# Performance work log

Hardware: AMD Instinct MI355X
Metric: run time of the kernel (lower is better)

Reference implementation:

```python
import jax, jax.numpy as jnp
import numpy as np

EPS = 1e-3  # Keras LayerNormalization default epsilon


def setup_inputs() -> dict:
    key = jax.random.key(0)
    ks = jax.random.split(key, 10)
    B, S, D, U = 4, 4096, 1024, 1024
    sc_in = 1.0 / np.sqrt(D)
    sc_u = 1.0 / np.sqrt(U)
    return {
        "inputs": jax.random.normal(ks[0], (B, S, D), dtype=jnp.float32),
        "w1": jax.random.normal(ks[1], (D, U), dtype=jnp.float32) * sc_in,
        "b1": jnp.zeros((U,), dtype=jnp.float32),
        "w2": jax.random.normal(ks[2], (U, U), dtype=jnp.float32) * sc_u,
        "b2": jnp.zeros((U,), dtype=jnp.float32),
        "wg": jax.random.normal(ks[3], (D, U), dtype=jnp.float32) * sc_in,
        "bg": jnp.zeros((U,), dtype=jnp.float32),
        "ws": jax.random.normal(ks[4], (D, U), dtype=jnp.float32) * sc_in,
        "bs": jnp.zeros((U,), dtype=jnp.float32),
        "gamma": jnp.ones((U,), dtype=jnp.float32),
        "beta": jnp.zeros((U,), dtype=jnp.float32),
    }


def reference(inputs, w1, b1, w2, b2, wg, bg, ws, bs, gamma, beta):
    # hidden branch: Dense(relu) -> (dropout inactive at inference) -> Dense
    h = jax.nn.relu(jnp.einsum('bsd,du->bsu', inputs, w1) + b1)
    x = jnp.einsum('bsu,uv->bsv', h, w2) + b2
    # gate on raw inputs
    g = jax.nn.sigmoid(jnp.einsum('bsd,du->bsu', inputs, wg) + bg)
    # skip projection
    s = jnp.einsum('bsd,du->bsu', inputs, ws) + bs
    y = x * g + s
    # LayerNormalization over last axis (Keras default eps=1e-3)
    mu = jnp.mean(y, axis=-1, keepdims=True)
    var = jnp.mean(jnp.square(y - mu), axis=-1, keepdims=True)
    return (y - mu) * jax.lax.rsqrt(var + EPS) * gamma + beta
```

## Files before the change

### kernel.cpp

```cpp
#include <hip/hip_runtime.h>
#include <hip/hip_bf16.h>

typedef short short8 __attribute__((ext_vector_type(8)));
typedef float f32x4 __attribute__((ext_vector_type(4)));

#define M_TOT 16384
#define NDIM  1024
#define BM 256
#define BN 256
#define BK 64
#define KH 32
#define NT (NDIM / BK)

static __device__ __forceinline__ unsigned short f2bf(float f) {
  unsigned int u = __builtin_bit_cast(unsigned int, f);
  unsigned int r = (u + 0x7fffu + ((u >> 16) & 1u)) >> 16;
  return (unsigned short)r;
}
static __device__ __forceinline__ float bf2f(unsigned short u) {
  return __builtin_bit_cast(float, ((unsigned int)u) << 16);
}

#define CLB() asm volatile("" ::: "memory")

__global__ __launch_bounds__(256) void cast_in(const float* __restrict__ in,
                                               unsigned short* __restrict__ out,
                                               int n4) {
  int i = blockIdx.x * 256 + threadIdx.x;
  if (i >= n4) return;
  float4 v = reinterpret_cast<const float4*>(in)[i];
  ushort4 o;
  o.x = f2bf(v.x); o.y = f2bf(v.y); o.z = f2bf(v.z); o.w = f2bf(v.w);
  reinterpret_cast<ushort4*>(out)[i] = o;
}

__global__ __launch_bounds__(256) void tcast(const float* __restrict__ src,
                                             unsigned short* __restrict__ dst) {
  __shared__ unsigned short tile[32][33];
  int bx = blockIdx.x * 32, by = blockIdx.y * 32;
  int x = threadIdx.x & 31, y = threadIdx.x >> 5;
#pragma unroll
  for (int i = 0; i < 32; i += 8)
    tile[y + i][x] = f2bf(src[(size_t)(by + y + i) * NDIM + bx + x]);
  __syncthreads();
#pragma unroll
  for (int i = 0; i < 32; i += 8)
    dst[(size_t)(bx + y + i) * NDIM + by + x] = tile[x][y + i];
}

template <int MODE>
__global__ __launch_bounds__(512, 2) void gemm256(
    const unsigned short* __restrict__ A,
    const unsigned short* __restrict__ Bt,
    const float* __restrict__ bias,
    unsigned short* __restrict__ O,
    const unsigned short* __restrict__ G,
    const unsigned short* __restrict__ S) {
  __shared__ __align__(16) unsigned short lds[2][2][2][256][KH];

  const int tid = threadIdx.x;
  const int lane = tid & 63;
  const int wave = tid >> 6;
  const int wm = wave >> 2;
  const int wn = wave & 3;

  const int id = blockIdx.x;
  const int xcd = id & 7;
  const int slot = id >> 3;
  const int rblk = xcd + 8 * (slot >> 2);
  const int cblk = slot & 3;
  const int m0 = rblk * BM, n0 = cblk * BN;

  const unsigned short* gA = A + (size_t)m0 * NDIM;
  const unsigned short* gB = Bt + (size_t)n0 * NDIM;

  f32x4 acc[8][4] = {};

  auto stage = [&](int buf, int mat, int h, const unsigned short* gsrc, int kt) {
#pragma unroll
    for (int j = 0; j < 2; ++j) {
      int cid = j * 512 + tid;
      int row = cid >> 2;
      int cs = cid & 3;
      int c = cs ^ ((row >> 1) & 3);
      const unsigned short* g = gsrc + (size_t)row * NDIM + kt * BK + h * KH + c * 8;
      unsigned short* l = &lds[buf][mat][h][0][0] + (size_t)(j * 512 + (tid & ~63)) * 8;
      __builtin_amdgcn_global_load_lds(
          (__attribute__((address_space(1))) void*)g,
          (__attribute__((address_space(3))) void*)l, 16, 0, 0);
    }
  };

  auto ldA = [&](short8* dst, int buf, int mih, int kk) {
#pragma unroll
    for (int mi = 0; mi < 4; ++mi) {
      int row = wm * 128 + (mih * 4 + mi) * 16 + (lane & 15);
      int cs = (lane >> 4) ^ ((row >> 1) & 3);
      dst[mi] = *reinterpret_cast<const short8*>(&lds[buf][0][kk][row][cs * 8]);
    }
  };
  auto ldB = [&](short8* dst, int buf, int kk) {
#pragma unroll
    for (int nj = 0; nj < 4; ++nj) {
      int row = wn * 64 + nj * 16 + (lane & 15);
      int cs = (lane >> 4) ^ ((row >> 1) & 3);
      dst[nj] = *reinterpret_cast<const short8*>(&lds[buf][1][kk][row][cs * 8]);
    }
  };

#define MFMA_Q(A4, B4, MI0)                                               \
  do {                                                                    \
    _Pragma("unroll") for (int mi = 0; mi < 4; ++mi)                      \
    _Pragma("unroll") for (int nj = 0; nj < 4; ++nj)                      \
      acc[MI0 + mi][nj] = __builtin_amdgcn_mfma_f32_16x16x32_bf16(        \
          A4[mi], B4[nj], acc[MI0 + mi][nj], 0, 0, 0);                    \
  } while (0)

#define BAR() do { CLB(); __builtin_amdgcn_s_barrier(); CLB(); } while (0)

  stage(0, 0, 0, gA, 0);
  stage(0, 1, 0, gB, 0);
  stage(0, 0, 1, gA, 0);
  stage(0, 1, 1, gB, 0);
  asm volatile("s_waitcnt vmcnt(4)" ::: "memory");
  BAR();

  short8 a_[4], b0_[4], b1_[4];

#pragma unroll 2
  for (int t = 0; t < NT; ++t) {
    const int cur = t & 1, nxt = cur ^ 1;
    const int ktn = (t < NT - 1) ? t + 1 : t;

    stage(nxt, 0, 0, gA, ktn);
    ldA(a_, cur, 0, 0);
    ldB(b0_, cur, 0);
    BAR();
    __builtin_amdgcn_s_setprio(1);
    MFMA_Q(a_, b0_, 0);
    __builtin_amdgcn_s_setprio(0);
    BAR();

    stage(nxt, 1, 0, gB, ktn);
    ldA(a_, cur, 1, 0);
    BAR();
    __builtin_amdgcn_s_setprio(1);
    MFMA_Q(a_, b0_, 4);
    __builtin_amdgcn_s_setprio(0);
    asm volatile("s_waitcnt vmcnt(4)" ::: "memory");
    BAR();

    stage(nxt, 0, 1, gA, ktn);
    ldA(a_, cur, 0, 1);
    ldB(b1_, cur, 1);
    BAR();
    __builtin_amdgcn_s_setprio(1);
    MFMA_Q(a_, b1_, 0);
    __builtin_amdgcn_s_setprio(0);
    BAR();

    stage(nxt, 1, 1, gB, ktn);
    ldA(a_, cur, 1, 1);
    BAR();
    __builtin_amdgcn_s_setprio(1);
    MFMA_Q(a_, b1_, 4);
    __builtin_amdgcn_s_setprio(0);
    asm volatile("s_waitcnt vmcnt(4)" ::: "memory");
    BAR();
  }

  const int crow0 = m0 + wm * 128;
  const int ccol0 = n0 + wn * 64;
#pragma unroll
  for (int mi = 0; mi < 8; ++mi) {
#pragma unroll
    for (int nj = 0; nj < 4; ++nj) {
      int row = crow0 + mi * 16 + ((lane >> 4) << 2);
      int col = ccol0 + nj * 16 + (lane & 15);
      float bc = bias[col];
#pragma unroll
      for (int r = 0; r < 4; ++r) {
        float v = acc[mi][nj][r] + bc;
        size_t idx = (size_t)(row + r) * NDIM + col;
        if (MODE == 0) {
          O[idx] = f2bf(fmaxf(v, 0.f));
        } else if (MODE == 1) {
          O[idx] = f2bf(1.f / (1.f + __expf(-v)));
        } else if (MODE == 2) {
          O[idx] = f2bf(v);
        } else {
          O[idx] = f2bf(v * bf2f(G[idx]) + bf2f(S[idx]));
        }
      }
    }
  }
#undef MFMA_Q
#undef BAR
}

__global__ __launch_bounds__(256) void layernorm_bf(
    const unsigned short* __restrict__ Ybf, float* __restrict__ Out,
    const float* __restrict__ gamma, const float* __restrict__ beta) {
  const int tid = threadIdx.x;
  const unsigned short* y = Ybf + (size_t)blockIdx.x * NDIM;
  ushort4 u = reinterpret_cast<const ushort4*>(y)[tid];
  float v0 = bf2f(u.x), v1 = bf2f(u.y), v2 = bf2f(u.z), v3 = bf2f(u.w);
  float s1 = v0 + v1 + v2 + v3;
  float s2 = v0 * v0 + v1 * v1 + v2 * v2 + v3 * v3;
#pragma unroll
  for (int o = 32; o > 0; o >>= 1) {
    s1 += __shfl_down(s1, o, 64);
    s2 += __shfl_down(s2, o, 64);
  }
  __shared__ float red[8];
  int wave = tid >> 6, lane = tid & 63;
  if (lane == 0) { red[wave] = s1; red[wave + 4] = s2; }
  __syncthreads();
  float S1 = red[0] + red[1] + red[2] + red[3];
  float S2 = red[4] + red[5] + red[6] + red[7];
  float mu = S1 * (1.f / NDIM);
  float var = S2 * (1.f / NDIM) - mu * mu;
  float inv = rsqrtf(var + 1e-3f);
  float4 gm = reinterpret_cast<const float4*>(gamma)[tid];
  float4 bt = reinterpret_cast<const float4*>(beta)[tid];
  float4 o;
  o.x = (v0 - mu) * inv * gm.x + bt.x;
  o.y = (v1 - mu) * inv * gm.y + bt.y;
  o.z = (v2 - mu) * inv * gm.z + bt.z;
  o.w = (v3 - mu) * inv * gm.w + bt.w;
  reinterpret_cast<float4*>(Out + (size_t)blockIdx.x * NDIM)[tid] = o;
}

extern "C" void kernel_launch(void* const* d_in, const int* in_sizes, int n_in,
                              void* d_out, int out_size, void* d_ws, size_t ws_size,
                              hipStream_t stream) {
  const float* inp = (const float*)d_in[0];
  const float* w1 = (const float*)d_in[1];
  const float* b1 = (const float*)d_in[2];
  const float* w2 = (const float*)d_in[3];
  const float* b2 = (const float*)d_in[4];
  const float* wg = (const float*)d_in[5];
  const float* bg = (const float*)d_in[6];
  const float* wsk = (const float*)d_in[7];
  const float* bs = (const float*)d_in[8];
  const float* gamma = (const float*)d_in[9];
  const float* beta = (const float*)d_in[10];

  char* p = (char*)d_ws;
  const size_t act_bf16 = (size_t)M_TOT * NDIM * 2;
  const size_t w_bf16 = (size_t)NDIM * NDIM * 2;
  unsigned short* Ain = (unsigned short*)p; p += act_bf16;
  unsigned short* H   = (unsigned short*)p; p += act_bf16;
  unsigned short* G   = (unsigned short*)p; p += act_bf16;
  unsigned short* S   = (unsigned short*)p; p += act_bf16;
  unsigned short* Ybf = (unsigned short*)p; p += act_bf16;
  unsigned short* W1t = (unsigned short*)p; p += w_bf16;
  unsigned short* W2t = (unsigned short*)p; p += w_bf16;
  unsigned short* Wgt = (unsigned short*)p; p += w_bf16;
  unsigned short* Wst = (unsigned short*)p; p += w_bf16;

  cast_in<<<(M_TOT * NDIM / 4 + 255) / 256, 256, 0, stream>>>(inp, Ain, M_TOT * NDIM / 4);
  dim3 tg(32, 32);
  tcast<<<tg, 256, 0, stream>>>(w1, W1t);
  tcast<<<tg, 256, 0, stream>>>(w2, W2t);
  tcast<<<tg, 256, 0, stream>>>(wg, Wgt);
  tcast<<<tg, 256, 0, stream>>>(wsk, Wst);

  const int nblk = (M_TOT / BM) * (NDIM / BN);
  gemm256<0><<<nblk, 512, 0, stream>>>(Ain, W1t, b1, H, nullptr, nullptr);
  gemm256<1><<<nblk, 512, 0, stream>>>(Ain, Wgt, bg, G, nullptr, nullptr);
  gemm256<2><<<nblk, 512, 0, stream>>>(Ain, Wst, bs, S, nullptr, nullptr);
  gemm256<3><<<nblk, 512, 0, stream>>>(H, W2t, b2, Ybf, G, S);
  layernorm_bf<<<M_TOT, 256, 0, stream>>>(Ybf, (float*)d_out, gamma, beta);
}
```

Measured before the change: 207.2 us.

## Restructure GEMM mainloop into 4-stage BK=32 pipeline with one barrier per step

Replaces the double-buffered BK=64 mainloop, which used four barrier-separated quarter phases, with a four-slot ring of BK=32 tiles. Each slot is loaded three steps ahead and there is a single barrier per k-step, with the last tiles drained explicitly at the end. The goal is deeper prefetch and fewer barriers so that global-to-LDS latency hides behind MFMA work. In exchange each step does less MFMA work per barrier, and holding 8 A fragments at once raises register pressure.

```diff
diff --git a/kernel.cpp b/kernel.cpp
--- a/kernel.cpp
+++ b/kernel.cpp
@@ -8,8 +8,7 @@
 #define NDIM  1024
 #define BM 256
 #define BN 256
-#define BK 64
-#define KH 32
+#define BK 32
 #define NT (NDIM / BK)
 
 static __device__ __forceinline__ unsigned short f2bf(float f) {
@@ -56,7 +55,7 @@
     unsigned short* __restrict__ O,
     const unsigned short* __restrict__ G,
     const unsigned short* __restrict__ S) {
-  __shared__ __align__(16) unsigned short lds[2][2][2][256][KH];
+  __shared__ __align__(16) unsigned short lds[4][2][256][BK];
 
   const int tid = threadIdx.x;
   const int lane = tid & 63;
@@ -66,9 +65,9 @@
 
   const int id = blockIdx.x;
   const int xcd = id & 7;
-  const int slot = id >> 3;
-  const int rblk = xcd + 8 * (slot >> 2);
-  const int cblk = slot & 3;
+  const int slot0 = id >> 3;
+  const int rblk = xcd + 8 * (slot0 >> 2);
+  const int cblk = slot0 & 3;
   const int m0 = rblk * BM, n0 = cblk * BN;
 
   const unsigned short* gA = A + (size_t)m0 * NDIM;
@@ -76,98 +75,75 @@
 
   f32x4 acc[8][4] = {};
 
-  auto stage = [&](int buf, int mat, int h, const unsigned short* gsrc, int kt) {
-#pragma unroll
-    for (int j = 0; j < 2; ++j) {
-      int cid = j * 512 + tid;
-      int row = cid >> 2;
-      int cs = cid & 3;
-      int c = cs ^ ((row >> 1) & 3);
-      const unsigned short* g = gsrc + (size_t)row * NDIM + kt * BK + h * KH + c * 8;
-      unsigned short* l = &lds[buf][mat][h][0][0] + (size_t)(j * 512 + (tid & ~63)) * 8;
+  auto stage = [&](int slot, int kt) {
+#pragma unroll
+    for (int q = 0; q < 4; ++q) {
+      int cid = q * 512 + tid;
+      int mat = q >> 1;
+      int local = cid & 1023;
+      int row = local >> 2;
+      int c = (local & 3) ^ ((row >> 1) & 3);
+      const unsigned short* g =
+          (mat ? gB : gA) + (size_t)row * NDIM + kt * BK + c * 8;
+      unsigned short* l = &lds[slot][mat][0][0] +
+                          (size_t)((q * 512 + (tid & ~63)) & 1023) * 8;
       __builtin_amdgcn_global_load_lds(
           (__attribute__((address_space(1))) void*)g,
           (__attribute__((address_space(3))) void*)l, 16, 0, 0);
     }
   };
 
-  auto ldA = [&](short8* dst, int buf, int mih, int kk) {
-#pragma unroll
-    for (int mi = 0; mi < 4; ++mi) {
-      int row = wm * 128 + (mih * 4 + mi) * 16 + (lane & 15);
-      int cs = (lane >> 4) ^ ((row >> 1) & 3);
-      dst[mi] = *reinterpret_cast<const short8*>(&lds[buf][0][kk][row][cs * 8]);
-    }
-  };
-  auto ldB = [&](short8* dst, int buf, int kk) {
+  auto compute = [&](int slot) {
+    short8 af[8], bf[4];
 #pragma unroll
     for (int nj = 0; nj < 4; ++nj) {
       int row = wn * 64 + nj * 16 + (lane & 15);
       int cs = (lane >> 4) ^ ((row >> 1) & 3);
-      dst[nj] = *reinterpret_cast<const short8*>(&lds[buf][1][kk][row][cs * 8]);
-    }
+      bf[nj] = *reinterpret_cast<const short8*>(&lds[slot][1][row][cs * 8]);
+    }
+#pragma unroll
+    for (int mi = 0; mi < 8; ++mi) {
+      int row = wm * 128 + mi * 16 + (lane & 15);
+      int cs = (lane >> 4) ^ ((row >> 1) & 3);
+      af[mi] = *reinterpret_cast<const short8*>(&lds[slot][0][row][cs * 8]);
+    }
+    __builtin_amdgcn_s_setprio(1);
+#pragma unroll
+    for (int mi = 0; mi < 8; ++mi)
+#pragma unroll
+      for (int nj = 0; nj < 4; ++nj)
+        acc[mi][nj] = __builtin_amdgcn_mfma_f32_16x16x32_bf16(
+            af[mi], bf[nj], acc[mi][nj], 0, 0, 0);
+    __builtin_amdgcn_s_setprio(0);
   };
 
-#define MFMA_Q(A4, B4, MI0)                                               \
-  do {                                                                    \
-    _Pragma("unroll") for (int mi = 0; mi < 4; ++mi)                      \
-    _Pragma("unroll") for (int nj = 0; nj < 4; ++nj)                      \
-      acc[MI0 + mi][nj] = __builtin_amdgcn_mfma_f32_16x16x32_bf16(        \
-          A4[mi], B4[nj], acc[MI0 + mi][nj], 0, 0, 0);                    \
-  } while (0)
-
+#define VMW(N) asm volatile("s_waitcnt vmcnt(" #N ")" ::: "memory")
 #define BAR() do { CLB(); __builtin_amdgcn_s_barrier(); CLB(); } while (0)
 
-  stage(0, 0, 0, gA, 0);
-  stage(0, 1, 0, gB, 0);
-  stage(0, 0, 1, gA, 0);
-  stage(0, 1, 1, gB, 0);
-  asm volatile("s_waitcnt vmcnt(4)" ::: "memory");
-  BAR();
-
-  short8 a_[4], b0_[4], b1_[4];
-
-#pragma unroll 2
-  for (int t = 0; t < NT; ++t) {
-    const int cur = t & 1, nxt = cur ^ 1;
-    const int ktn = (t < NT - 1) ? t + 1 : t;
-
-    stage(nxt, 0, 0, gA, ktn);
-    ldA(a_, cur, 0, 0);
-    ldB(b0_, cur, 0);
-    BAR();
-    __builtin_amdgcn_s_setprio(1);
-    MFMA_Q(a_, b0_, 0);
-    __builtin_amdgcn_s_setprio(0);
-    BAR();
-
-    stage(nxt, 1, 0, gB, ktn);
-    ldA(a_, cur, 1, 0);
-    BAR();
-    __builtin_amdgcn_s_setprio(1);
-    MFMA_Q(a_, b0_, 4);
-    __builtin_amdgcn_s_setprio(0);
-    asm volatile("s_waitcnt vmcnt(4)" ::: "memory");
-    BAR();
-
-    stage(nxt, 0, 1, gA, ktn);
-    ldA(a_, cur, 0, 1);
-    ldB(b1_, cur, 1);
-    BAR();
-    __builtin_amdgcn_s_setprio(1);
-    MFMA_Q(a_, b1_, 0);
-    __builtin_amdgcn_s_setprio(0);
-    BAR();
-
-    stage(nxt, 1, 1, gB, ktn);
-    ldA(a_, cur, 1, 1);
-    BAR();
-    __builtin_amdgcn_s_setprio(1);
-    MFMA_Q(a_, b1_, 4);
-    __builtin_amdgcn_s_setprio(0);
-    asm volatile("s_waitcnt vmcnt(4)" ::: "memory");
+  stage(0, 0);
+  stage(1, 1);
+  stage(2, 2);
+  VMW(8);
+  BAR();
+
+#pragma unroll 4
+  for (int t = 0; t < NT - 4; ++t) {
+    stage((t + 3) & 3, t + 3);
+    compute(t & 3);
+    VMW(8);
     BAR();
   }
+  stage(3, 31);
+  compute(0);
+  VMW(8);
+  BAR();
+  compute(1);
+  VMW(4);
+  BAR();
+  compute(2);
+  VMW(0);
+  BAR();
+  compute(3);
 
   const int crow0 = m0 + wm * 128;
   const int ccol0 = n0 + wn * 64;
@@ -194,7 +170,7 @@
       }
     }
   }
-#undef MFMA_Q
+#undef VMW
 #undef BAR
 }
 
```

Result: faster. 201.6 us (-2.7%).
